# Kernel tuning notes

Measured on AMD Instinct MI355X. Metric: run time of the kernel, lower is better.

Reference implementation:

```python
import jax, jax.numpy as jnp
import numpy as np

B, S, CIN, H, W, D = 8, 16, 128, 64, 64, 64


def setup_inputs() -> dict:
    key = jax.random.key(0)
    ks = jax.random.split(key, 16)
    def rn(i, shape, s=0.05):
        return jax.random.normal(ks[i], shape, dtype=jnp.float32) * s
    z = lambda *sh: jnp.zeros(sh, jnp.float32)
    return {
        "x": jax.random.normal(ks[0], (B, S, CIN, H, W), dtype=jnp.float32),
        "proj_w": rn(1, (D, CIN, 1, 1)),
        "bn_gamma": jnp.ones((D,), jnp.float32),
        "bn_beta": z(D),
        "clstm_w": rn(2, (4 * D, 2 * D, 3, 3)),
        "clstm_b": z(4 * D),
        "lq_wih": rn(3, (4 * D, D)), "lq_whh": rn(4, (4 * D, D)),
        "lq_bih": z(4 * D), "lq_bhh": z(4 * D),
        "lr_wih": rn(5, (4 * D, D)), "lr_whh": rn(6, (4 * D, D)),
        "lr_bih": z(4 * D), "lr_bhh": z(4 * D),
        "fcf_w": rn(7, (D, D)), "fcf_b": z(D),
        "fcF_w": rn(8, (D, D)), "fcF_b": z(D),
        "fcQ_w": rn(9, (D, D)), "fcQ_b": z(D),
        "fcR_w": rn(10, (D, D)), "fcR_b": z(D),
        "P_init": 0.1 * jnp.eye(D, dtype=jnp.float32),
        "fc_w": rn(11, (D, D)), "fc_b": z(D),
        "fco_w": rn(12, (1, D)), "fco_b": z(1),
        "fca_w": rn(13, (1, D)), "fca_b": z(1),
    }


def _fc(zv, w, b):
    return zv @ w.T + b


def _forward(x, proj_w, bn_gamma, bn_beta, clstm_w, clstm_b,
             lq_wih, lq_whh, lq_bih, lq_bhh, lr_wih, lr_whh, lr_bih, lr_bhh,
             fcf_w, fcf_b, fcF_w, fcF_b, fcQ_w, fcQ_b, fcR_w, fcR_b,
             P_init, fc_w, fc_b, fco_w, fco_b, fca_w, fca_b):
    Bv, Sv, C, Hv, Wv = x.shape
    Dv = P_init.shape[0]
    # 1x1 projection conv + BatchNorm2d (training-mode batch statistics)
    y = x.reshape(Bv * Sv, C, Hv, Wv)
    y = jax.lax.conv_general_dilated(y, proj_w, (1, 1), "VALID")
    mu = y.mean((0, 2, 3), keepdims=True)
    var = ((y - mu) ** 2).mean((0, 2, 3), keepdims=True)
    y = (y - mu) * jax.lax.rsqrt(var + 1e-5)
    y = y * bn_gamma[None, :, None, None] + bn_beta[None, :, None, None]
    xp = y.reshape(Bv, Sv, Dv, Hv, Wv)
    x0 = xp[:, 0]  # forward uses x[:, 0] as innovation target every step
    eye = jnp.eye(Dv, dtype=x.dtype)

    def convlstm(inp, h, c):
        zc = jax.lax.conv_general_dilated(jnp.concatenate([inp, h], axis=1), clstm_w, (1, 1), "SAME")
        zc = zc + clstm_b[None, :, None, None]
        i, f, o, g = jnp.split(zc, 4, axis=1)
        c2 = jax.nn.sigmoid(f) * c + jax.nn.sigmoid(i) * jnp.tanh(g)
        return jax.nn.sigmoid(o) * jnp.tanh(c2), c2

    def lstm_cell(zv, h, c, wih, whh, bih, bhh):  # pytorch gate order i,f,g,o
        g = zv @ wih.T + h @ whh.T + bih + bhh
        i, f, gg, o = jnp.split(g, 4, axis=-1)
        c2 = jax.nn.sigmoid(f) * c + jax.nn.sigmoid(i) * jnp.tanh(gg)
        return jax.nn.sigmoid(o) * jnp.tanh(c2), c2

    def step(carry, xs):
        y_hat, hf, cf, hQ, cQ, hR, cR, P = carry
        hf, cf = convlstm(y_hat, hf, cf)            # [B,D,H,W]
        lf = jnp.transpose(hf, (0, 2, 3, 1))        # [B,H,W,D]
        y_tick = jnp.transpose(_fc(lf, fcf_w, fcf_b), (0, 3, 1, 2))
        Fv = _fc(hf.mean((2, 3)), fcF_w, fcF_b)     # [B,D]
        FF = Fv[:, :, None] * Fv[:, None, :]        # outer product F F^T
        hQ, cQ = lstm_cell(y_tick.mean((2, 3)), hQ, cQ, lq_wih, lq_whh, lq_bih, lq_bhh)
        Qm = jnp.exp(_fc(hQ, fcQ_w, fcQ_b))[:, :, None] * eye
        hR, cR = lstm_cell(xs.mean((2, 3)), hR, cR, lr_wih, lr_whh, lr_bih, lr_bhh)
        Rm = jnp.exp(_fc(hR, fcR_w, fcR_b))[:, :, None] * eye
        P = P * FF + Qm
        K = P @ jnp.linalg.inv(P + Rm)
        IK = eye - K
        P = IK @ P @ jnp.swapaxes(IK, 1, 2) + K @ Rm @ jnp.swapaxes(K, 1, 2)
        v = x0 - y_tick
        y_hat = y_tick + jnp.einsum("bij,bjhw->bihw", K, v)
        return (y_hat, hf, cf, hQ, cQ, hR, cR, P), y_hat

    z2 = jnp.zeros((Bv, Dv, Hv, Wv), x.dtype)
    z1 = jnp.zeros((Bv, Dv), x.dtype)
    P0 = jnp.broadcast_to(P_init, (Bv, Dv, Dv))
    carry0 = (x0, z2, z2, z1, z1, z1, z1, P0)
    _, ys = jax.lax.scan(step, carry0, jnp.transpose(xp, (1, 0, 2, 3, 4)))
    feat = jnp.transpose(ys, (1, 0, 2, 3, 4)).mean((3, 4))  # [B,S,D] adaptive avgpool
    feat = jax.nn.relu(_fc(feat, fc_w, fc_b))
    offset = _fc(feat, fco_w, fco_b)
    angle = _fc(feat, fca_w, fca_b)
    return offset, angle


def reference(x, proj_w, bn_gamma, bn_beta, clstm_w, clstm_b,
              lq_wih, lq_whh, lq_bih, lq_bhh, lr_wih, lr_whh, lr_bih, lr_bhh,
              fcf_w, fcf_b, fcF_w, fcF_b, fcQ_w, fcQ_b, fcR_w, fcR_b,
              P_init, fc_w, fc_b, fco_w, fco_b, fca_w, fca_b):
    return _forward(x, proj_w, bn_gamma, bn_beta, clstm_w, clstm_b,
                    lq_wih, lq_whh, lq_bih, lq_bhh, lr_wih, lr_whh, lr_bih, lr_bhh,
                    fcf_w, fcf_b, fcF_w, fcF_b, fcQ_w, fcQ_b, fcR_w, fcR_b,
                    P_init, fc_w, fc_b, fco_w, fco_b, fca_w, fca_b)
```

## Files before the change

kernel.cpp:

```cpp
#include <hip/hip_runtime.h>
#include <math.h>


__device__ __forceinline__ float sigf(float x){ return 1.0f/(1.0f + expf(-x)); }

#define FMA4(A, W, V0, V1, V2, V3) { (A).x += (W)*(V0); (A).y += (W)*(V1); (A).z += (W)*(V2); (A).w += (W)*(V3); }

__global__ __launch_bounds__(256) void k_w4(const float* __restrict__ cw, const float* __restrict__ fcf_w,
                                            float* __restrict__ w4, float* __restrict__ fwT){
    int idx = blockIdx.x*256 + threadIdx.x;
    if (idx < 294912){
        int col = idx & 255;
        int rk  = idx >> 8;
        int w = col >> 5, g = (col >> 3) & 3, c = col & 7;
        int oc = g*64 + w*8 + c;
        w4[idx] = cw[oc*1152 + rk];
    } else if (idx < 294912 + 4096){
        int i = idx - 294912;
        int ch = i >> 6, dp = i & 63;
        fwT[i] = fcf_w[dp*64 + ch];
    }
}

__global__ __launch_bounds__(256) void k_proj(const float* __restrict__ x, const float* __restrict__ pw,
                                              float* __restrict__ x0raw, float* __restrict__ psum,
                                              float* __restrict__ psumsq){
    __shared__ __align__(16) float smem[8192];
    const int tile = blockIdx.x;
    const int n    = blockIdx.y;
    const int tid  = threadIdx.x;
    const int pj = tid & 63, dg = tid >> 6;

    for (int r = tid; r < 8192; r += 256){
        int c = r >> 6, d = r & 63;
        smem[r] = pw[d*128 + c];
    }
    __syncthreads();

    const int p0 = tile*256 + pj*4;
    float4 acc[16];
#pragma unroll
    for (int i=0;i<16;i++) acc[i] = make_float4(0.f,0.f,0.f,0.f);

    const float* xb = x + (((size_t)n) << 19) + p0;
    for (int c = 0; c < 128; ++c){
        float4 xv = *(const float4*)(xb + ((size_t)c << 12));
        const float4* wr = (const float4*)(smem + c*64 + dg*16);
#pragma unroll
        for (int q=0;q<4;++q){
            float4 w4 = wr[q];
            FMA4(acc[q*4+0], w4.x, xv.x, xv.y, xv.z, xv.w);
            FMA4(acc[q*4+1], w4.y, xv.x, xv.y, xv.z, xv.w);
            FMA4(acc[q*4+2], w4.z, xv.x, xv.y, xv.z, xv.w);
            FMA4(acc[q*4+3], w4.w, xv.x, xv.y, xv.z, xv.w);
        }
    }

    const int t = n & 15, b = n >> 4;
    if (t == 0){
#pragma unroll
        for (int i=0;i<16;i++){
            int dd = dg*16 + i;
            *(float4*)(x0raw + (((size_t)(b*64 + dd)) << 12) + p0) = acc[i];
        }
    }
    float ls[16], lss[16];
#pragma unroll
    for (int i=0;i<16;i++){
        float4 a = acc[i];
        ls[i]  = a.x + a.y + a.z + a.w;
        lss[i] = a.x*a.x + a.y*a.y + a.z*a.z + a.w*a.w;
    }
    __syncthreads();
#pragma unroll
    for (int i=0;i<16;i++) smem[pj*65 + dg*16 + i] = ls[i];
    __syncthreads();
    if (tid < 64){
        float s = 0.f;
        for (int p=0;p<64;p++) s += smem[p*65 + tid];
        psum[((n*16 + tile) << 6) + tid] = s;
    }
    __syncthreads();
#pragma unroll
    for (int i=0;i<16;i++) smem[pj*65 + dg*16 + i] = lss[i];
    __syncthreads();
    if (tid < 64){
        float s = 0.f;
        for (int p=0;p<64;p++) s += smem[p*65 + tid];
        psumsq[((n*16 + tile) << 6) + tid] = s;
    }
}

__global__ __launch_bounds__(64) void k_bnfinal(const float* __restrict__ psum, const float* __restrict__ psumsq,
                                                const float* __restrict__ gamma, const float* __restrict__ beta,
                                                float* __restrict__ scale, float* __restrict__ shift,
                                                float* __restrict__ xmean){
    const int d = threadIdx.x;
    double gs = 0.0, gss = 0.0;
    for (int n=0;n<128;n++){
        float s = 0.f, ss = 0.f;
        for (int tl=0;tl<16;tl++){
            s  += psum  [((n*16+tl)<<6) + d];
            ss += psumsq[((n*16+tl)<<6) + d];
        }
        gs += (double)s; gss += (double)ss;
    }
    double mu  = gs  / 524288.0;
    double var = gss / 524288.0 - mu*mu;
    double sc  = (double)gamma[d] / sqrt(var + 1e-5);
    float scf = (float)sc;
    float shf = (float)((double)beta[d] - mu*sc);
    scale[d] = scf; shift[d] = shf;
    for (int n=0;n<128;n++){
        float s = 0.f;
        for (int tl=0;tl<16;tl++) s += psum[((n*16+tl)<<6) + d];
        xmean[(n<<6) + d] = (s * (1.f/4096.f)) * scf + shf;
    }
}

__global__ __launch_bounds__(256) void k_zero(float* __restrict__ z){
    size_t i = ((size_t)blockIdx.x*256 + threadIdx.x)*4;
    *(float4*)(z + i) = make_float4(0.f,0.f,0.f,0.f);
}

__global__ __launch_bounds__(256) void k_init(const float* __restrict__ scale, const float* __restrict__ shift,
                                              float* __restrict__ x0, float* __restrict__ yhat_p,
                                              const float* __restrict__ Pinit, float* __restrict__ Pg,
                                              float* __restrict__ hQ, float* __restrict__ cQ,
                                              float* __restrict__ hR, float* __restrict__ cR){
    size_t idx = (size_t)blockIdx.x*256 + threadIdx.x;
    int d = (int)((idx >> 12) & 63);
    float v = x0[idx]*scale[d] + shift[d];
    x0[idx] = v;
    int b = (int)(idx >> 18), r = (int)((idx >> 6) & 63), xx = (int)(idx & 63);
    yhat_p[(((size_t)(b*64 + d))*66 + r + 1)*72 + xx + 4] = v;
    if (idx < 512){ hQ[idx]=0.f; cQ[idx]=0.f; hR[idx]=0.f; cR[idx]=0.f; }
    if (idx < 32768) Pg[idx] = Pinit[idx & 4095];
}

__global__ __launch_bounds__(512) void k_conv(const float* __restrict__ yhat_p, const float* __restrict__ hfin_p,
                                              float* __restrict__ hfout_p, float* __restrict__ cf,
                                              const float* __restrict__ w4, const float* __restrict__ cb,
                                              const float* __restrict__ fwT, const float* __restrict__ fcf_b,
                                              float* __restrict__ ytick,
                                              float* __restrict__ hfpart, float* __restrict__ ytpartR){
    __shared__ __align__(16) float smem[9184];
    const int HL = 864, YL = 5024;
    const int row = blockIdx.x;
    const int b   = blockIdx.y;
    const int tid = threadIdx.x;
    const int px  = tid & 63;
    const int w   = __builtin_amdgcn_readfirstlane(tid >> 6);

    float acc[4][8];
#pragma unroll
    for (int g=0;g<4;++g)
#pragma unroll
        for (int c=0;c<8;++c) acc[g][c] = 0.f;

    int s_icl=0, s_r=0, s_x4=0;
    if (tid < 216){
        s_icl = tid/54; int rem = tid - s_icl*54; s_r = rem/18; s_x4 = rem - s_r*18;
    }

    for (int icc = 0; icc < 32; ++icc){
        __syncthreads();
        if (tid < 216){
            int ic = icc*4 + s_icl;
            const float* f = (ic < 64) ? yhat_p : hfin_p;
            *(float4*)(smem + tid*4) =
                *(const float4*)(f + (((size_t)(b*64 + (ic & 63)))*66 + row + s_r)*72 + s_x4*4);
        }
        __syncthreads();
#pragma unroll 1
        for (int icl = 0; icl < 4; ++icl){
            const float* ib = smem + icl*216 + px + 3;
            const float v0 = ib[0],   v1 = ib[1],   v2 = ib[2];
            const float v3 = ib[72],  v4 = ib[73],  v5 = ib[74];
            const float v6 = ib[144], v7 = ib[145], v8 = ib[146];
            const float* wp = w4 + ((size_t)(icc*36 + icl*9) << 8) + w*32;
#define WG(KI, VAL) { const float* q_ = wp + (KI)*256; \
    _Pragma("unroll") for (int g=0;g<4;++g) \
    _Pragma("unroll") for (int c=0;c<8;++c) acc[g][c] += q_[g*8+c]*(VAL); }
            WG(0,v0) WG(1,v1) WG(2,v2)
            WG(3,v3) WG(4,v4) WG(5,v5)
            WG(6,v6) WG(7,v7) WG(8,v8)
#undef WG
        }
    }

#pragma unroll
    for (int c=0;c<8;++c){
        const int d = w*8 + c;
        const float biv = cb[d], bfv = cb[64+d], bov = cb[128+d], bgv = cb[192+d];
        const size_t gidx = (((size_t)(b*64 + d)) << 12) + row*64 + px;
        float c_old = cf[gidx];
        float c2 = sigf(acc[1][c]+bfv)*c_old + sigf(acc[0][c]+biv)*tanhf(acc[3][c]+bgv);
        float hh = sigf(acc[2][c]+bov)*tanhf(c2);
        cf[gidx] = c2;
        hfout_p[(((size_t)(b*64 + d))*66 + row + 1)*72 + px + 4] = hh;
        smem[HL + d*65 + px] = hh;
    }
    __syncthreads();

    float yt[8];
#pragma unroll
    for (int j=0;j<8;++j) yt[j] = fcf_b[w*8 + j];
    for (int ch = 0; ch < 64; ++ch){
        float hv = smem[HL + ch*65 + px];
        const float* fp = fwT + ch*64 + w*8;
#pragma unroll
        for (int j=0;j<8;++j) yt[j] += fp[j]*hv;
    }
#pragma unroll
    for (int j=0;j<8;++j){
        const int dp = w*8 + j;
        ytick[(((size_t)(b*64 + dp)) << 12) + row*64 + px] = yt[j];
        smem[YL + dp*65 + px] = yt[j];
    }
    __syncthreads();
    if (tid < 64){
        float s = 0.f, s2 = 0.f;
#pragma unroll 8
        for (int pxx=0; pxx<64; ++pxx){
            s  += smem[HL + tid*65 + pxx];
            s2 += smem[YL + tid*65 + pxx];
        }
        hfpart [((b*64 + row) << 6) + tid] = s;
        ytpartR[((b*64 + row) << 6) + tid] = s2;
    }
}

__global__ __launch_bounds__(256) void k_small(int t,
        const float* __restrict__ hfpart, const float* __restrict__ ytpartR, const float* __restrict__ xmean,
        const float* __restrict__ fcF_w, const float* __restrict__ fcF_b,
        const float* __restrict__ lq_wih, const float* __restrict__ lq_whh,
        const float* __restrict__ lq_bih, const float* __restrict__ lq_bhh,
        const float* __restrict__ lr_wih, const float* __restrict__ lr_whh,
        const float* __restrict__ lr_bih, const float* __restrict__ lr_bhh,
        const float* __restrict__ fcQ_w, const float* __restrict__ fcQ_b,
        const float* __restrict__ fcR_w, const float* __restrict__ fcR_b,
        float* __restrict__ hQ, float* __restrict__ cQ, float* __restrict__ hR, float* __restrict__ cR,
        float* __restrict__ Pg, float* __restrict__ Kg){
    const int b = blockIdx.x, tid = threadIdx.x;
    __shared__ __align__(16) float aug[64*132];
    __shared__ __align__(16) float Pl[4096];
    __shared__ float hfm[64], ytm[64], xm[64], Fv[64], Qd[64], Rd[64], rds[64];
    __shared__ float hq_s[64], cq_s[64], hr_s[64], cr_s[64];
    __shared__ float gq[256], gr[256];

    if (tid < 64){
        float s = 0.f;
        for (int r=0;r<64;r++) s += hfpart[((b*64 + r) << 6) + tid];
        hfm[tid] = s * (1.f/4096.f);
        float s2 = 0.f;
        for (int r=0;r<64;r++) s2 += ytpartR[((b*64 + r) << 6) + tid];
        ytm[tid] = s2 * (1.f/4096.f);
        xm[tid] = xmean[((b*16 + t) << 6) + tid];
        hq_s[tid] = hQ[b*64+tid]; cq_s[tid] = cQ[b*64+tid];
        hr_s[tid] = hR[b*64+tid]; cr_s[tid] = cR[b*64+tid];
    }
    __syncthreads();
    {
        int j = tid;
        float aq = lq_bih[j] + lq_bhh[j];
        float ar = lr_bih[j] + lr_bhh[j];
        for (int e=0;e<64;e++){
            aq += lq_wih[j*64+e]*ytm[e] + lq_whh[j*64+e]*hq_s[e];
            ar += lr_wih[j*64+e]*xm[e]  + lr_whh[j*64+e]*hr_s[e];
        }
        gq[j] = aq; gr[j] = ar;
    }
    if (tid < 64){
        float a = fcF_b[tid];
        for (int e=0;e<64;e++) a += fcF_w[tid*64+e]*hfm[e];
        Fv[tid] = a;
    }
    __syncthreads();
    if (tid < 64){
        int dd = tid;
        float gi = gq[dd], gf = gq[64+dd], gg = gq[128+dd], go = gq[192+dd];
        float c2 = sigf(gf)*cq_s[dd] + sigf(gi)*tanhf(gg);
        float h2 = sigf(go)*tanhf(c2);
        cq_s[dd] = c2; hq_s[dd] = h2;
        gi = gr[dd]; gf = gr[64+dd]; gg = gr[128+dd]; go = gr[192+dd];
        c2 = sigf(gf)*cr_s[dd] + sigf(gi)*tanhf(gg);
        h2 = sigf(go)*tanhf(c2);
        cr_s[dd] = c2; hr_s[dd] = h2;
    }
    __syncthreads();
    if (tid < 64){
        float aq_ = fcQ_b[tid], ar_ = fcR_b[tid];
        for (int e=0;e<64;e++){ aq_ += fcQ_w[tid*64+e]*hq_s[e]; ar_ += fcR_w[tid*64+e]*hr_s[e]; }
        Qd[tid] = expf(aq_); Rd[tid] = expf(ar_);
        hQ[b*64+tid] = hq_s[tid]; cQ[b*64+tid] = cq_s[tid];
        hR[b*64+tid] = hr_s[tid]; cR[b*64+tid] = cr_s[tid];
    }
    __syncthreads();
    for (int r = tid; r < 4096; r += 256){
        int i = r >> 6, j = r & 63;
        float p = Pg[((size_t)b << 12) + r] * Fv[i]*Fv[j] + (i==j ? Qd[i] : 0.f);
        Pl[r] = p;
        aug[i*132 + 64 + j] = p;
        aug[i*132 + j]      = p + (i==j ? Rd[i] : 0.f);
    }
    __syncthreads();
    const int r_ = tid & 63, cq_ = tid >> 6;
    for (int k = 0; k < 64; ++k){
        float akk = aug[k*132 + k];
        float f = aug[r_*132 + k] / akk;
        if (r_ != k){
#pragma unroll
            for (int u = 0; u < 8; ++u){
                int c4 = cq_*32 + u*4;
                if (c4 + 3 > k){
                    float4 pv = *(const float4*)(aug + k*132 + c4);
                    float4 av = *(const float4*)(aug + r_*132 + c4);
                    av.x = (c4+0 > k) ? av.x - f*pv.x : av.x;
                    av.y = (c4+1 > k) ? av.y - f*pv.y : av.y;
                    av.z = (c4+2 > k) ? av.z - f*pv.z : av.z;
                    av.w = (c4+3 > k) ? av.w - f*pv.w : av.w;
                    *(float4*)(aug + r_*132 + c4) = av;
                }
            }
        }
        __syncthreads();
    }
    if (tid < 64) rds[tid] = 1.0f / aug[tid*132 + tid];
    __syncthreads();
    {
        const int i = tid >> 2, jq = tid & 3;
        float4 tv[4];
#pragma unroll
        for (int q=0;q<4;++q) tv[q] = *(const float4*)(Pl + i*64 + jq*16 + q*4);
        for (int m=0;m<64;++m){
            float kim = aug[m*132 + 64 + i] * rds[m];
#pragma unroll
            for (int q=0;q<4;++q){
                float4 pv = *(const float4*)(Pl + m*64 + jq*16 + q*4);
                tv[q].x -= kim*pv.x; tv[q].y -= kim*pv.y; tv[q].z -= kim*pv.z; tv[q].w -= kim*pv.w;
            }
        }
#pragma unroll
        for (int q=0;q<4;++q) *(float4*)(aug + i*132 + jq*16 + q*4) = tv[q];
    }
    __syncthreads();
    {
        const int i = tid >> 2, jq = tid & 3;
        float4 a2[4];
#pragma unroll
        for (int q=0;q<4;++q) a2[q] = *(const float4*)(aug + i*132 + jq*16 + q*4);
        for (int m=0;m<64;++m){
            float t1im = aug[i*132 + m];
            float kim  = aug[m*132 + 64 + i] * rds[m];
            float coef = rds[m] * (kim * Rd[m] - t1im);
#pragma unroll
            for (int q=0;q<4;++q){
                float4 yv = *(const float4*)(aug + m*132 + 64 + jq*16 + q*4);
                a2[q].x += coef*yv.x; a2[q].y += coef*yv.y; a2[q].z += coef*yv.z; a2[q].w += coef*yv.w;
            }
        }
        size_t base = ((size_t)b << 12) + (size_t)i*64;
#pragma unroll
        for (int q=0;q<4;++q) *(float4*)(Pg + base + jq*16 + q*4) = a2[q];
#pragma unroll
        for (int q=0;q<4;++q){
#pragma unroll
            for (int e=0;e<4;++e){
                int j = jq*16 + q*4 + e;
                Kg[base + j] = aug[j*132 + 64 + i] * rds[j];
            }
        }
    }
}

__global__ __launch_bounds__(256) void k_apply(int t, const float* __restrict__ ytick,
                                               const float* __restrict__ x0, const float* __restrict__ Kg,
                                               float* __restrict__ yhat_p, float* __restrict__ featpart){
    __shared__ __align__(16) float kt[4160];
    const int tile = blockIdx.x;
    const int b    = blockIdx.y;
    const int tid  = threadIdx.x;
    const int pj = tid & 31, dgp = tid >> 5;

    for (int r = tid; r < 4096; r += 256){
        int i = r >> 6, j = r & 63;
        kt[j*65 + i] = Kg[((size_t)b << 12) + r];
    }
    __syncthreads();

    const int p0 = tile*128 + pj*4;
    const int rr = p0 >> 6, xx = p0 & 63;
    float4 acc[8];
#pragma unroll
    for (int i=0;i<8;i++) acc[i] = make_float4(0.f,0.f,0.f,0.f);

    for (int j = 0; j < 64; ++j){
        size_t gi = (((size_t)(b*64 + j)) << 12) + p0;
        float4 xv = *(const float4*)(x0 + gi);
        float4 yv = *(const float4*)(ytick + gi);
        float u0 = xv.x - yv.x, u1 = xv.y - yv.y, u2 = xv.z - yv.z, u3 = xv.w - yv.w;
        const float* kr = kt + j*65 + dgp*8;
#pragma unroll
        for (int il=0; il<8; ++il){
            float kv = kr[il];
            FMA4(acc[il], kv, u0,u1,u2,u3);
        }
    }
    float ls[8];
#pragma unroll
    for (int il=0;il<8;++il){
        int d = dgp*8 + il;
        size_t gi = (((size_t)(b*64 + d)) << 12) + p0;
        float4 yv = *(const float4*)(ytick + gi);
        float4 o;
        o.x = yv.x + acc[il].x; o.y = yv.y + acc[il].y; o.z = yv.z + acc[il].z; o.w = yv.w + acc[il].w;
        *(float4*)(yhat_p + (((size_t)(b*64 + d))*66 + rr + 1)*72 + xx + 4) = o;
        ls[il] = o.x + o.y + o.z + o.w;
    }
    __syncthreads();
#pragma unroll
    for (int il=0;il<8;++il) kt[pj*65 + dgp*8 + il] = ls[il];
    __syncthreads();
    if (tid < 64){
        float s = 0.f;
        for (int q=0;q<32;++q) s += kt[q*65 + tid];
        featpart[(((size_t)((t*8 + b)*32 + tile)) << 6) + tid] = s;
    }
}

__global__ __launch_bounds__(64) void k_head(const float* __restrict__ featpart,
                                             const float* __restrict__ fc_w, const float* __restrict__ fc_b,
                                             const float* __restrict__ fco_w, const float* __restrict__ fco_b,
                                             const float* __restrict__ fca_w, const float* __restrict__ fca_b,
                                             float* __restrict__ out){
    const int bt = blockIdx.x;
    const int b = bt >> 4, t = bt & 15;
    __shared__ float fs[64];
    const int i = threadIdx.x;
    float s = 0.f;
    for (int tile=0;tile<32;tile++) s += featpart[(((size_t)((t*8 + b)*32 + tile)) << 6) + i];
    fs[i] = s * (1.f/4096.f);
    __syncthreads();
    float a = fc_b[i];
    for (int e=0;e<64;e++) a += fc_w[i*64+e]*fs[e];
    a = fmaxf(a, 0.f);
    float po = a * fco_w[i];
    float pa = a * fca_w[i];
    for (int off=32; off; off >>= 1){ po += __shfl_down(po, off); pa += __shfl_down(pa, off); }
    if (i == 0){
        out[bt]       = po + fco_b[0];
        out[128 + bt] = pa + fca_b[0];
    }
}

extern "C" void kernel_launch(void* const* d_in, const int* in_sizes, int n_in,
                              void* d_out, int out_size, void* d_ws, size_t ws_size,
                              hipStream_t stream){
    const float* x       = (const float*)d_in[0];
    const float* proj_w  = (const float*)d_in[1];
    const float* bn_g    = (const float*)d_in[2];
    const float* bn_b    = (const float*)d_in[3];
    const float* clstm_w = (const float*)d_in[4];
    const float* clstm_b = (const float*)d_in[5];
    const float* lq_wih  = (const float*)d_in[6];
    const float* lq_whh  = (const float*)d_in[7];
    const float* lq_bih  = (const float*)d_in[8];
    const float* lq_bhh  = (const float*)d_in[9];
    const float* lr_wih  = (const float*)d_in[10];
    const float* lr_whh  = (const float*)d_in[11];
    const float* lr_bih  = (const float*)d_in[12];
    const float* lr_bhh  = (const float*)d_in[13];
    const float* fcf_w   = (const float*)d_in[14];
    const float* fcf_b   = (const float*)d_in[15];
    const float* fcF_w   = (const float*)d_in[16];
    const float* fcF_b   = (const float*)d_in[17];
    const float* fcQ_w   = (const float*)d_in[18];
    const float* fcQ_b   = (const float*)d_in[19];
    const float* fcR_w   = (const float*)d_in[20];
    const float* fcR_b   = (const float*)d_in[21];
    const float* P_init  = (const float*)d_in[22];
    const float* fc_w    = (const float*)d_in[23];
    const float* fc_b    = (const float*)d_in[24];
    const float* fco_w   = (const float*)d_in[25];
    const float* fco_b   = (const float*)d_in[26];
    const float* fca_w   = (const float*)d_in[27];
    const float* fca_b   = (const float*)d_in[28];
    float* out = (float*)d_out;
    float* ws  = (float*)d_ws;

    const size_t PF    = 2433024;
    const size_t FIELD = 2097152;
    float* yhat_p = ws;
    float* hfA_p  = ws + PF;
    float* hfB_p  = ws + 2*PF;
    float* cf     = ws + 3*PF;
    float* x0     = cf + FIELD;
    float* ytick  = x0 + FIELD;
    float* w4     = ytick + FIELD;
    float* fwT    = w4 + 294912;
    float* psum   = fwT + 4096;
    float* psumsq = psum + 131072;
    float* scale  = psumsq + 131072;
    float* shift  = scale + 64;
    float* xmean  = shift + 64;
    float* hfpart = xmean + 8192;
    float* ytpartR= hfpart + 32768;
    float* featpart = ytpartR + 32768;
    float* hQ     = featpart + 262144;
    float* cQ     = hQ + 512;
    float* hR     = cQ + 512;
    float* cR     = hR + 512;
    float* Pg     = cR + 512;
    float* Kg     = Pg + 32768;

    hipLaunchKernelGGL(k_w4, dim3(1168), dim3(256), 0, stream, clstm_w, fcf_w, w4, fwT);
    hipLaunchKernelGGL(k_proj, dim3(16,128), dim3(256), 0, stream, x, proj_w, x0, psum, psumsq);
    hipLaunchKernelGGL(k_bnfinal, dim3(1), dim3(64), 0, stream, psum, psumsq, bn_g, bn_b, scale, shift, xmean);
    hipLaunchKernelGGL(k_zero, dim3(9176), dim3(256), 0, stream, ws);
    hipLaunchKernelGGL(k_init, dim3(8192), dim3(256), 0, stream, scale, shift, x0, yhat_p, P_init, Pg, hQ, cQ, hR, cR);

    for (int t = 0; t < 16; ++t){
        float* hf_in  = (t & 1) ? hfB_p : hfA_p;
        float* hf_out = (t & 1) ? hfA_p : hfB_p;
        hipLaunchKernelGGL(k_conv, dim3(64,8), dim3(512), 0, stream,
                           yhat_p, hf_in, hf_out, cf, w4, clstm_b,
                           fwT, fcf_b, ytick, hfpart, ytpartR);
        hipLaunchKernelGGL(k_small, dim3(8), dim3(256), 0, stream, t,
                           hfpart, ytpartR, xmean, fcF_w, fcF_b,
                           lq_wih, lq_whh, lq_bih, lq_bhh,
                           lr_wih, lr_whh, lr_bih, lr_bhh,
                           fcQ_w, fcQ_b, fcR_w, fcR_b,
                           hQ, cQ, hR, cR, Pg, Kg);
        hipLaunchKernelGGL(k_apply, dim3(32,8), dim3(256), 0, stream, t,
                           ytick, x0, Kg, yhat_p, featpart);
    }
    hipLaunchKernelGGL(k_head, dim3(128), dim3(64), 0, stream,
                       featpart, fc_w, fc_b, fco_w, fco_b, fca_w, fca_b, out);
}
```

Baseline: 5.719 ms.

## Fold fcf projection into Kalman update matrix and split conv output channels across blocks

```diff
diff --git a/kernel.cpp b/kernel.cpp
--- a/kernel.cpp
+++ b/kernel.cpp
@@ -6,19 +6,15 @@
 
 #define FMA4(A, W, V0, V1, V2, V3) { (A).x += (W)*(V0); (A).y += (W)*(V1); (A).z += (W)*(V2); (A).w += (W)*(V3); }
 
-__global__ __launch_bounds__(256) void k_w4(const float* __restrict__ cw, const float* __restrict__ fcf_w,
-                                            float* __restrict__ w4, float* __restrict__ fwT){
+__global__ __launch_bounds__(256) void k_w5(const float* __restrict__ cw, float* __restrict__ w5){
     int idx = blockIdx.x*256 + threadIdx.x;
     if (idx < 294912){
-        int col = idx & 255;
-        int rk  = idx >> 8;
-        int w = col >> 5, g = (col >> 3) & 3, c = col & 7;
-        int oc = g*64 + w*8 + c;
-        w4[idx] = cw[oc*1152 + rk];
-    } else if (idx < 294912 + 4096){
-        int i = idx - 294912;
-        int ch = i >> 6, dp = i & 63;
-        fwT[i] = fcf_w[dp*64 + ch];
+        int col = idx & 127;
+        int rkh = idx >> 7;
+        int chh = rkh & 1, rk = rkh >> 1;
+        int w = col >> 4, g = (col >> 2) & 3, c = col & 3;
+        int oc = g*64 + chh*32 + w*4 + c;
+        w5[idx] = cw[oc*1152 + rk];
     }
 }
 
@@ -140,99 +136,87 @@
 
 __global__ __launch_bounds__(512) void k_conv(const float* __restrict__ yhat_p, const float* __restrict__ hfin_p,
                                               float* __restrict__ hfout_p, float* __restrict__ cf,
-                                              const float* __restrict__ w4, const float* __restrict__ cb,
-                                              const float* __restrict__ fwT, const float* __restrict__ fcf_b,
-                                              float* __restrict__ ytick,
-                                              float* __restrict__ hfpart, float* __restrict__ ytpartR){
-    __shared__ __align__(16) float smem[9184];
-    const int HL = 864, YL = 5024;
+                                              const float* __restrict__ w5, const float* __restrict__ cb,
+                                              float* __restrict__ hfpart){
+    __shared__ __align__(16) float smem[6912];
     const int row = blockIdx.x;
-    const int b   = blockIdx.y;
+    const int chh = blockIdx.y;
+    const int b   = blockIdx.z;
     const int tid = threadIdx.x;
     const int px  = tid & 63;
     const int w   = __builtin_amdgcn_readfirstlane(tid >> 6);
-
-    float acc[4][8];
+    const int c0  = chh*32 + w*4;
+
+    float acc[4][4];
 #pragma unroll
     for (int g=0;g<4;++g)
 #pragma unroll
-        for (int c=0;c<8;++c) acc[g][c] = 0.f;
-
-    int s_icl=0, s_r=0, s_x4=0;
-    if (tid < 216){
-        s_icl = tid/54; int rem = tid - s_icl*54; s_r = rem/18; s_x4 = rem - s_r*18;
-    }
-
-    for (int icc = 0; icc < 32; ++icc){
-        __syncthreads();
-        if (tid < 216){
-            int ic = icc*4 + s_icl;
-            const float* f = (ic < 64) ? yhat_p : hfin_p;
-            *(float4*)(smem + tid*4) =
-                *(const float4*)(f + (((size_t)(b*64 + (ic & 63)))*66 + row + s_r)*72 + s_x4*4);
-        }
-        __syncthreads();
-#pragma unroll 1
-        for (int icl = 0; icl < 4; ++icl){
-            const float* ib = smem + icl*216 + px + 3;
+        for (int c=0;c<4;++c) acc[g][c] = 0.f;
+
+    int s_icl0, s_r0, s_x40, s_icl1=0, s_r1=0, s_x41=0;
+    { int s = tid; s_icl0 = s/54; int rem = s - s_icl0*54; s_r0 = rem/18; s_x40 = rem - s_r0*18; }
+    const bool has1 = (tid < 352);
+    if (has1){ int s = tid + 512; s_icl1 = s/54; int rem = s - s_icl1*54; s_r1 = rem/18; s_x41 = rem - s_r1*18; }
+
+    float4 pf0, pf1;
+    auto issue = [&](int icc){
+        { int ic = icc*16 + s_icl0; const float* f = (ic < 64) ? yhat_p : hfin_p;
+          pf0 = *(const float4*)(f + (((size_t)(b*64 + (ic & 63)))*66 + row + s_r0)*72 + s_x40*4); }
+        if (has1){ int ic = icc*16 + s_icl1; const float* f = (ic < 64) ? yhat_p : hfin_p;
+          pf1 = *(const float4*)(f + (((size_t)(b*64 + (ic & 63)))*66 + row + s_r1)*72 + s_x41*4); }
+    };
+    auto commit = [&](int buf){
+        *(float4*)(smem + buf*3456 + tid*4) = pf0;
+        if (has1) *(float4*)(smem + buf*3456 + (tid+512)*4) = pf1;
+    };
+
+    issue(0); commit(0); __syncthreads();
+    int p = 0;
+    for (int icc = 0; icc < 8; ++icc){
+        if (icc < 7) issue(icc+1);
+        const float* ib0 = smem + p*3456;
+#pragma unroll 2
+        for (int icl = 0; icl < 16; ++icl){
+            const float* ib = ib0 + icl*216 + px + 3;
             const float v0 = ib[0],   v1 = ib[1],   v2 = ib[2];
             const float v3 = ib[72],  v4 = ib[73],  v5 = ib[74];
             const float v6 = ib[144], v7 = ib[145], v8 = ib[146];
-            const float* wp = w4 + ((size_t)(icc*36 + icl*9) << 8) + w*32;
-#define WG(KI, VAL) { const float* q_ = wp + (KI)*256; \
+            const int rk = (icc*16 + icl)*9;
+#define WG(KI, VAL) { const float* q_ = w5 + ((((size_t)(rk+(KI)))*2 + chh) << 7) + w*16; \
     _Pragma("unroll") for (int g=0;g<4;++g) \
-    _Pragma("unroll") for (int c=0;c<8;++c) acc[g][c] += q_[g*8+c]*(VAL); }
+    _Pragma("unroll") for (int c=0;c<4;++c) acc[g][c] += q_[g*4+c]*(VAL); }
             WG(0,v0) WG(1,v1) WG(2,v2)
             WG(3,v3) WG(4,v4) WG(5,v5)
             WG(6,v6) WG(7,v7) WG(8,v8)
 #undef WG
         }
-    }
-
-#pragma unroll
-    for (int c=0;c<8;++c){
-        const int d = w*8 + c;
-        const float biv = cb[d], bfv = cb[64+d], bov = cb[128+d], bgv = cb[192+d];
+        if (icc < 7) commit(p^1);
+        __syncthreads();
+        p ^= 1;
+    }
+
+#pragma unroll
+    for (int c=0;c<4;++c){
+        const int d = c0 + c;
+        float zi = acc[0][c] + cb[d];
+        float zf = acc[1][c] + cb[64+d];
+        float zo = acc[2][c] + cb[128+d];
+        float zg = acc[3][c] + cb[192+d];
         const size_t gidx = (((size_t)(b*64 + d)) << 12) + row*64 + px;
         float c_old = cf[gidx];
-        float c2 = sigf(acc[1][c]+bfv)*c_old + sigf(acc[0][c]+biv)*tanhf(acc[3][c]+bgv);
-        float hh = sigf(acc[2][c]+bov)*tanhf(c2);
+        float c2 = sigf(zf)*c_old + sigf(zi)*tanhf(zg);
+        float hh = sigf(zo)*tanhf(c2);
         cf[gidx] = c2;
         hfout_p[(((size_t)(b*64 + d))*66 + row + 1)*72 + px + 4] = hh;
-        smem[HL + d*65 + px] = hh;
-    }
-    __syncthreads();
-
-    float yt[8];
-#pragma unroll
-    for (int j=0;j<8;++j) yt[j] = fcf_b[w*8 + j];
-    for (int ch = 0; ch < 64; ++ch){
-        float hv = smem[HL + ch*65 + px];
-        const float* fp = fwT + ch*64 + w*8;
-#pragma unroll
-        for (int j=0;j<8;++j) yt[j] += fp[j]*hv;
-    }
-#pragma unroll
-    for (int j=0;j<8;++j){
-        const int dp = w*8 + j;
-        ytick[(((size_t)(b*64 + dp)) << 12) + row*64 + px] = yt[j];
-        smem[YL + dp*65 + px] = yt[j];
-    }
-    __syncthreads();
-    if (tid < 64){
-        float s = 0.f, s2 = 0.f;
-#pragma unroll 8
-        for (int pxx=0; pxx<64; ++pxx){
-            s  += smem[HL + tid*65 + pxx];
-            s2 += smem[YL + tid*65 + pxx];
-        }
-        hfpart [((b*64 + row) << 6) + tid] = s;
-        ytpartR[((b*64 + row) << 6) + tid] = s2;
+        float hs = hh;
+        for (int off=32; off; off >>= 1) hs += __shfl_down(hs, off);
+        if (px == 0) hfpart[((b*64 + row) << 6) + d] = hs;
     }
 }
 
 __global__ __launch_bounds__(256) void k_small(int t,
-        const float* __restrict__ hfpart, const float* __restrict__ ytpartR, const float* __restrict__ xmean,
+        const float* __restrict__ hfpart, const float* __restrict__ xmean,
+        const float* __restrict__ fcf_w, const float* __restrict__ fcf_b,
         const float* __restrict__ fcF_w, const float* __restrict__ fcF_b,
         const float* __restrict__ lq_wih, const float* __restrict__ lq_whh,
         const float* __restrict__ lq_bih, const float* __restrict__ lq_bhh,
@@ -241,11 +225,12 @@
         const float* __restrict__ fcQ_w, const float* __restrict__ fcQ_b,
         const float* __restrict__ fcR_w, const float* __restrict__ fcR_b,
         float* __restrict__ hQ, float* __restrict__ cQ, float* __restrict__ hR, float* __restrict__ cR,
-        float* __restrict__ Pg, float* __restrict__ Kg){
+        float* __restrict__ Pg, float* __restrict__ Kg,
+        float* __restrict__ Mg, float* __restrict__ v0g){
     const int b = blockIdx.x, tid = threadIdx.x;
     __shared__ __align__(16) float aug[64*132];
     __shared__ __align__(16) float Pl[4096];
-    __shared__ float hfm[64], ytm[64], xm[64], Fv[64], Qd[64], Rd[64], rds[64];
+    __shared__ float hfm[64], ytm[64], xm[64], Fv[64], Qd[64], Rd[64], rds[64], fb_s[64];
     __shared__ float hq_s[64], cq_s[64], hr_s[64], cr_s[64];
     __shared__ float gq[256], gr[256];
 
@@ -253,12 +238,19 @@
         float s = 0.f;
         for (int r=0;r<64;r++) s += hfpart[((b*64 + r) << 6) + tid];
         hfm[tid] = s * (1.f/4096.f);
-        float s2 = 0.f;
-        for (int r=0;r<64;r++) s2 += ytpartR[((b*64 + r) << 6) + tid];
-        ytm[tid] = s2 * (1.f/4096.f);
         xm[tid] = xmean[((b*16 + t) << 6) + tid];
         hq_s[tid] = hQ[b*64+tid]; cq_s[tid] = cQ[b*64+tid];
         hr_s[tid] = hR[b*64+tid]; cr_s[tid] = cR[b*64+tid];
+        fb_s[tid] = fcf_b[tid];
+    }
+    __syncthreads();
+    if (tid < 64){
+        float a = fb_s[tid], a2 = fcF_b[tid];
+        for (int e=0;e<64;e++){
+            a  += fcf_w[tid*64+e]*hfm[e];
+            a2 += fcF_w[tid*64+e]*hfm[e];
+        }
+        ytm[tid] = a; Fv[tid] = a2;
     }
     __syncthreads();
     {
@@ -270,11 +262,6 @@
             ar += lr_wih[j*64+e]*xm[e]  + lr_whh[j*64+e]*hr_s[e];
         }
         gq[j] = aq; gr[j] = ar;
-    }
-    if (tid < 64){
-        float a = fcF_b[tid];
-        for (int e=0;e<64;e++) a += fcF_w[tid*64+e]*hfm[e];
-        Fv[tid] = a;
     }
     __syncthreads();
     if (tid < 64){
@@ -372,60 +359,86 @@
             }
         }
     }
-}
-
-__global__ __launch_bounds__(256) void k_apply(int t, const float* __restrict__ ytick,
-                                               const float* __restrict__ x0, const float* __restrict__ Kg,
+    __syncthreads();
+    for (int r = tid; r < 4096; r += 256) Pl[r] = fcf_w[r];
+    __syncthreads();
+    {
+        const int i = tid >> 2, jq = tid & 3;
+        float4 m4[4];
+#pragma unroll
+        for (int q=0;q<4;++q) m4[q] = *(const float4*)(Pl + i*64 + jq*16 + q*4);
+        float sv = fb_s[i];
+        for (int m=0;m<64;++m){
+            float kim = aug[m*132 + 64 + i] * rds[m];
+#pragma unroll
+            for (int q=0;q<4;++q){
+                float4 pv = *(const float4*)(Pl + m*64 + jq*16 + q*4);
+                m4[q].x -= kim*pv.x; m4[q].y -= kim*pv.y; m4[q].z -= kim*pv.z; m4[q].w -= kim*pv.w;
+            }
+            sv -= kim * fb_s[m];
+        }
+        size_t base = ((size_t)b << 12) + (size_t)i*64;
+#pragma unroll
+        for (int q=0;q<4;++q) *(float4*)(Mg + base + jq*16 + q*4) = m4[q];
+        if (jq == 0) v0g[b*64 + i] = sv;
+    }
+}
+
+__global__ __launch_bounds__(256) void k_apply(int t, const float* __restrict__ hf_p,
+                                               const float* __restrict__ x0,
+                                               const float* __restrict__ Kg, const float* __restrict__ Mg,
+                                               const float* __restrict__ v0g,
                                                float* __restrict__ yhat_p, float* __restrict__ featpart){
     __shared__ __align__(16) float kt[4160];
-    const int tile = blockIdx.x;
-    const int b    = blockIdx.y;
-    const int tid  = threadIdx.x;
-    const int pj = tid & 31, dgp = tid >> 5;
+    __shared__ __align__(16) float mt[4160];
+    const int row = blockIdx.x;
+    const int b   = blockIdx.y;
+    const int tid = threadIdx.x;
+    const int pj = tid & 15, dgp = tid >> 4;
 
     for (int r = tid; r < 4096; r += 256){
         int i = r >> 6, j = r & 63;
         kt[j*65 + i] = Kg[((size_t)b << 12) + r];
-    }
-    __syncthreads();
-
-    const int p0 = tile*128 + pj*4;
-    const int rr = p0 >> 6, xx = p0 & 63;
-    float4 acc[8];
-#pragma unroll
-    for (int i=0;i<8;i++) acc[i] = make_float4(0.f,0.f,0.f,0.f);
+        mt[j*65 + i] = Mg[((size_t)b << 12) + r];
+    }
+    __syncthreads();
+
+    const int px0 = pj*4;
+    const int d0  = dgp*4;
+    float4 acc[4];
+#pragma unroll
+    for (int i=0;i<4;i++) acc[i] = make_float4(0.f,0.f,0.f,0.f);
 
     for (int j = 0; j < 64; ++j){
-        size_t gi = (((size_t)(b*64 + j)) << 12) + p0;
-        float4 xv = *(const float4*)(x0 + gi);
-        float4 yv = *(const float4*)(ytick + gi);
-        float u0 = xv.x - yv.x, u1 = xv.y - yv.y, u2 = xv.z - yv.z, u3 = xv.w - yv.w;
-        const float* kr = kt + j*65 + dgp*8;
-#pragma unroll
-        for (int il=0; il<8; ++il){
-            float kv = kr[il];
-            FMA4(acc[il], kv, u0,u1,u2,u3);
-        }
-    }
-    float ls[8];
-#pragma unroll
-    for (int il=0;il<8;++il){
-        int d = dgp*8 + il;
-        size_t gi = (((size_t)(b*64 + d)) << 12) + p0;
-        float4 yv = *(const float4*)(ytick + gi);
-        float4 o;
-        o.x = yv.x + acc[il].x; o.y = yv.y + acc[il].y; o.z = yv.z + acc[il].z; o.w = yv.w + acc[il].w;
-        *(float4*)(yhat_p + (((size_t)(b*64 + d))*66 + rr + 1)*72 + xx + 4) = o;
+        float4 xv = *(const float4*)(x0 + (((size_t)(b*64 + j)) << 12) + row*64 + px0);
+        float4 hv = *(const float4*)(hf_p + (((size_t)(b*64 + j))*66 + row + 1)*72 + px0 + 4);
+        const float* kr = kt + j*65 + d0;
+        const float* mr = mt + j*65 + d0;
+#pragma unroll
+        for (int il=0; il<4; ++il){
+            FMA4(acc[il], kr[il], xv.x, xv.y, xv.z, xv.w);
+            FMA4(acc[il], mr[il], hv.x, hv.y, hv.z, hv.w);
+        }
+    }
+    float ls[4];
+#pragma unroll
+    for (int il=0;il<4;++il){
+        int d = d0 + il;
+        float v0v = v0g[b*64 + d];
+        float4 o = acc[il];
+        o.x += v0v; o.y += v0v; o.z += v0v; o.w += v0v;
+        *(float4*)(yhat_p + (((size_t)(b*64 + d))*66 + row + 1)*72 + px0 + 4) = o;
         ls[il] = o.x + o.y + o.z + o.w;
     }
     __syncthreads();
 #pragma unroll
-    for (int il=0;il<8;++il) kt[pj*65 + dgp*8 + il] = ls[il];
+    for (int il=0;il<4;++il) kt[pj*65 + d0 + il] = ls[il];
     __syncthreads();
     if (tid < 64){
         float s = 0.f;
-        for (int q=0;q<32;++q) s += kt[q*65 + tid];
-        featpart[(((size_t)((t*8 + b)*32 + tile)) << 6) + tid] = s;
+#pragma unroll
+        for (int q=0;q<16;++q) s += kt[q*65 + tid];
+        featpart[(((size_t)((t*8 + b)*64 + row)) << 6) + tid] = s;
     }
 }
 
@@ -439,7 +452,7 @@
     __shared__ float fs[64];
     const int i = threadIdx.x;
     float s = 0.f;
-    for (int tile=0;tile<32;tile++) s += featpart[(((size_t)((t*8 + b)*32 + tile)) << 6) + i];
+    for (int row=0;row<64;row++) s += featpart[(((size_t)((t*8 + b)*64 + row)) << 6) + i];
     fs[i] = s * (1.f/4096.f);
     __syncthreads();
     float a = fc_b[i];
@@ -496,25 +509,24 @@
     float* hfB_p  = ws + 2*PF;
     float* cf     = ws + 3*PF;
     float* x0     = cf + FIELD;
-    float* ytick  = x0 + FIELD;
-    float* w4     = ytick + FIELD;
-    float* fwT    = w4 + 294912;
-    float* psum   = fwT + 4096;
+    float* w5     = x0 + FIELD;
+    float* psum   = w5 + 294912;
     float* psumsq = psum + 131072;
     float* scale  = psumsq + 131072;
     float* shift  = scale + 64;
     float* xmean  = shift + 64;
     float* hfpart = xmean + 8192;
-    float* ytpartR= hfpart + 32768;
-    float* featpart = ytpartR + 32768;
-    float* hQ     = featpart + 262144;
+    float* featpart = hfpart + 32768;
+    float* hQ     = featpart + 524288;
     float* cQ     = hQ + 512;
     float* hR     = cQ + 512;
     float* cR     = hR + 512;
     float* Pg     = cR + 512;
     float* Kg     = Pg + 32768;
-
-    hipLaunchKernelGGL(k_w4, dim3(1168), dim3(256), 0, stream, clstm_w, fcf_w, w4, fwT);
+    float* Mg     = Kg + 32768;
+    float* v0g    = Mg + 32768;
+
+    hipLaunchKernelGGL(k_w5, dim3(1152), dim3(256), 0, stream, clstm_w, w5);
     hipLaunchKernelGGL(k_proj, dim3(16,128), dim3(256), 0, stream, x, proj_w, x0, psum, psumsq);
     hipLaunchKernelGGL(k_bnfinal, dim3(1), dim3(64), 0, stream, psum, psumsq, bn_g, bn_b, scale, shift, xmean);
     hipLaunchKernelGGL(k_zero, dim3(9176), dim3(256), 0, stream, ws);
@@ -523,17 +535,16 @@
     for (int t = 0; t < 16; ++t){
         float* hf_in  = (t & 1) ? hfB_p : hfA_p;
         float* hf_out = (t & 1) ? hfA_p : hfB_p;
-        hipLaunchKernelGGL(k_conv, dim3(64,8), dim3(512), 0, stream,
-                           yhat_p, hf_in, hf_out, cf, w4, clstm_b,
-                           fwT, fcf_b, ytick, hfpart, ytpartR);
+        hipLaunchKernelGGL(k_conv, dim3(64,2,8), dim3(512), 0, stream,
+                           yhat_p, hf_in, hf_out, cf, w5, clstm_b, hfpart);
         hipLaunchKernelGGL(k_small, dim3(8), dim3(256), 0, stream, t,
-                           hfpart, ytpartR, xmean, fcF_w, fcF_b,
+                           hfpart, xmean, fcf_w, fcf_b, fcF_w, fcF_b,
                            lq_wih, lq_whh, lq_bih, lq_bhh,
                            lr_wih, lr_whh, lr_bih, lr_bhh,
                            fcQ_w, fcQ_b, fcR_w, fcR_b,
-                           hQ, cQ, hR, cR, Pg, Kg);
-        hipLaunchKernelGGL(k_apply, dim3(32,8), dim3(256), 0, stream, t,
-                           ytick, x0, Kg, yhat_p, featpart);
+                           hQ, cQ, hR, cR, Pg, Kg, Mg, v0g);
+        hipLaunchKernelGGL(k_apply, dim3(64,8), dim3(256), 0, stream, t,
+                           hf_out, x0, Kg, Mg, v0g, yhat_p, featpart);
     }
     hipLaunchKernelGGL(k_head, dim3(128), dim3(64), 0, stream,
                        featpart, fc_w, fc_b, fco_w, fco_b, fca_w, fca_b, out);
```

Result: slower. 6.839 ms (+19.6%).

## Compute two output rows per ConvLSTM block with double-buffered input staging

Applied to the files above, without the earlier changes.

```diff
diff --git a/kernel.cpp b/kernel.cpp
--- a/kernel.cpp
+++ b/kernel.cpp
@@ -144,90 +144,123 @@
                                               const float* __restrict__ fwT, const float* __restrict__ fcf_b,
                                               float* __restrict__ ytick,
                                               float* __restrict__ hfpart, float* __restrict__ ytpartR){
-    __shared__ __align__(16) float smem[9184];
-    const int HL = 864, YL = 5024;
-    const int row = blockIdx.x;
+    __shared__ __align__(16) float smem[9216];
+    const int rp2 = blockIdx.x*2;
     const int b   = blockIdx.y;
     const int tid = threadIdx.x;
     const int px  = tid & 63;
     const int w   = __builtin_amdgcn_readfirstlane(tid >> 6);
 
-    float acc[4][8];
+    float acc[4][8][2];
 #pragma unroll
     for (int g=0;g<4;++g)
 #pragma unroll
-        for (int c=0;c<8;++c) acc[g][c] = 0.f;
-
-    int s_icl=0, s_r=0, s_x4=0;
-    if (tid < 216){
-        s_icl = tid/54; int rem = tid - s_icl*54; s_r = rem/18; s_x4 = rem - s_r*18;
-    }
-
-    for (int icc = 0; icc < 32; ++icc){
+        for (int c=0;c<8;++c){ acc[g][c][0]=0.f; acc[g][c][1]=0.f; }
+
+    int si[3], sr[3], sx[3];
+#pragma unroll
+    for (int j=0;j<3;++j){
+        int s = tid + j*512;
+        si[j] = s/72; int rem = s - si[j]*72; sr[j] = rem/18; sx[j] = rem - sr[j]*18;
+    }
+    const bool has2 = (tid < 128);
+
+    float4 pf[3];
+    auto issue = [&](int icc){
+#pragma unroll
+        for (int j=0;j<3;++j){
+            if (j == 2 && !has2) break;
+            int ic = icc*16 + si[j];
+            const float* f = (ic < 64) ? yhat_p : hfin_p;
+            pf[j] = *(const float4*)(f + (((size_t)(b*64 + (ic & 63)))*66 + rp2 + sr[j])*72 + sx[j]*4);
+        }
+    };
+    auto commit = [&](int buf){
+        *(float4*)(smem + buf*4608 + tid*4)          = pf[0];
+        *(float4*)(smem + buf*4608 + (tid+512)*4)    = pf[1];
+        if (has2) *(float4*)(smem + buf*4608 + (tid+1024)*4) = pf[2];
+    };
+
+    issue(0); commit(0); __syncthreads();
+    int p = 0;
+    for (int icc = 0; icc < 8; ++icc){
+        if (icc < 7) issue(icc+1);
+        const float* ib0 = smem + p*4608;
+#pragma unroll 1
+        for (int icl = 0; icl < 16; ++icl){
+            const float* ib = ib0 + icl*288 + px + 3;
+            float v[4][3];
+#pragma unroll
+            for (int r=0;r<4;++r){
+                v[r][0] = ib[r*72]; v[r][1] = ib[r*72+1]; v[r][2] = ib[r*72+2];
+            }
+            const int rk = (icc*16 + icl)*9;
+#pragma unroll
+            for (int ky=0;ky<3;++ky){
+#pragma unroll
+                for (int kx=0;kx<3;++kx){
+                    const float* q_ = w4 + ((size_t)(rk + ky*3 + kx) << 8) + w*32;
+                    const float v0 = v[ky][kx], v1 = v[ky+1][kx];
+#pragma unroll
+                    for (int g=0;g<4;++g)
+#pragma unroll
+                        for (int c=0;c<8;++c){
+                            float wv = q_[g*8+c];
+                            acc[g][c][0] += wv*v0;
+                            acc[g][c][1] += wv*v1;
+                        }
+                }
+            }
+        }
+        if (icc < 7) commit(p^1);
         __syncthreads();
-        if (tid < 216){
-            int ic = icc*4 + s_icl;
-            const float* f = (ic < 64) ? yhat_p : hfin_p;
-            *(float4*)(smem + tid*4) =
-                *(const float4*)(f + (((size_t)(b*64 + (ic & 63)))*66 + row + s_r)*72 + s_x4*4);
-        }
-        __syncthreads();
-#pragma unroll 1
-        for (int icl = 0; icl < 4; ++icl){
-            const float* ib = smem + icl*216 + px + 3;
-            const float v0 = ib[0],   v1 = ib[1],   v2 = ib[2];
-            const float v3 = ib[72],  v4 = ib[73],  v5 = ib[74];
-            const float v6 = ib[144], v7 = ib[145], v8 = ib[146];
-            const float* wp = w4 + ((size_t)(icc*36 + icl*9) << 8) + w*32;
-#define WG(KI, VAL) { const float* q_ = wp + (KI)*256; \
-    _Pragma("unroll") for (int g=0;g<4;++g) \
-    _Pragma("unroll") for (int c=0;c<8;++c) acc[g][c] += q_[g*8+c]*(VAL); }
-            WG(0,v0) WG(1,v1) WG(2,v2)
-            WG(3,v3) WG(4,v4) WG(5,v5)
-            WG(6,v6) WG(7,v7) WG(8,v8)
-#undef WG
-        }
+        p ^= 1;
     }
 
 #pragma unroll
     for (int c=0;c<8;++c){
         const int d = w*8 + c;
         const float biv = cb[d], bfv = cb[64+d], bov = cb[128+d], bgv = cb[192+d];
-        const size_t gidx = (((size_t)(b*64 + d)) << 12) + row*64 + px;
-        float c_old = cf[gidx];
-        float c2 = sigf(acc[1][c]+bfv)*c_old + sigf(acc[0][c]+biv)*tanhf(acc[3][c]+bgv);
-        float hh = sigf(acc[2][c]+bov)*tanhf(c2);
-        cf[gidx] = c2;
-        hfout_p[(((size_t)(b*64 + d))*66 + row + 1)*72 + px + 4] = hh;
-        smem[HL + d*65 + px] = hh;
-    }
-    __syncthreads();
-
-    float yt[8];
-#pragma unroll
-    for (int j=0;j<8;++j) yt[j] = fcf_b[w*8 + j];
+#pragma unroll
+        for (int r=0;r<2;++r){
+            const size_t gidx = (((size_t)(b*64 + d)) << 12) + (rp2+r)*64 + px;
+            float c_old = cf[gidx];
+            float c2 = sigf(acc[1][c][r]+bfv)*c_old + sigf(acc[0][c][r]+biv)*tanhf(acc[3][c][r]+bgv);
+            float hh = sigf(acc[2][c][r]+bov)*tanhf(c2);
+            cf[gidx] = c2;
+            hfout_p[(((size_t)(b*64 + d))*66 + rp2 + r + 1)*72 + px + 4] = hh;
+            smem[d*130 + r*64 + px] = hh;
+            float hs = hh;
+            for (int off=32; off; off >>= 1) hs += __shfl_down(hs, off);
+            if (px == 0) hfpart[((b*64 + rp2 + r) << 6) + d] = hs;
+        }
+    }
+    __syncthreads();
+
+    float yt[2][8];
+#pragma unroll
+    for (int j=0;j<8;++j){ yt[0][j] = fcf_b[w*8 + j]; yt[1][j] = yt[0][j]; }
     for (int ch = 0; ch < 64; ++ch){
-        float hv = smem[HL + ch*65 + px];
+        float hv0 = smem[ch*130 + px];
+        float hv1 = smem[ch*130 + 64 + px];
         const float* fp = fwT + ch*64 + w*8;
 #pragma unroll
-        for (int j=0;j<8;++j) yt[j] += fp[j]*hv;
+        for (int j=0;j<8;++j){
+            float fv = fp[j];
+            yt[0][j] += fv*hv0;
+            yt[1][j] += fv*hv1;
+        }
     }
 #pragma unroll
     for (int j=0;j<8;++j){
         const int dp = w*8 + j;
-        ytick[(((size_t)(b*64 + dp)) << 12) + row*64 + px] = yt[j];
-        smem[YL + dp*65 + px] = yt[j];
-    }
-    __syncthreads();
-    if (tid < 64){
-        float s = 0.f, s2 = 0.f;
-#pragma unroll 8
-        for (int pxx=0; pxx<64; ++pxx){
-            s  += smem[HL + tid*65 + pxx];
-            s2 += smem[YL + tid*65 + pxx];
-        }
-        hfpart [((b*64 + row) << 6) + tid] = s;
-        ytpartR[((b*64 + row) << 6) + tid] = s2;
+#pragma unroll
+        for (int r=0;r<2;++r){
+            ytick[(((size_t)(b*64 + dp)) << 12) + (rp2+r)*64 + px] = yt[r][j];
+            float ys = yt[r][j];
+            for (int off=32; off; off >>= 1) ys += __shfl_down(ys, off);
+            if (px == 0) ytpartR[((b*64 + rp2 + r) << 6) + dp] = ys;
+        }
     }
 }
 
@@ -523,7 +556,7 @@
     for (int t = 0; t < 16; ++t){
         float* hf_in  = (t & 1) ? hfB_p : hfA_p;
         float* hf_out = (t & 1) ? hfA_p : hfB_p;
-        hipLaunchKernelGGL(k_conv, dim3(64,8), dim3(512), 0, stream,
+        hipLaunchKernelGGL(k_conv, dim3(32,8), dim3(512), 0, stream,
                            yhat_p, hf_in, hf_out, cf, w4, clstm_b,
                            fwT, fcf_b, ytick, hfpart, ytpartR);
         hipLaunchKernelGGL(k_small, dim3(8), dim3(256), 0, stream, t,
```

After: 7.880 ms. 37.8% more time.
